# Optimization experiments

Measured on AMD Instinct MI355X. Metric: run time of the kernel, lower is better.

## Reference

```python
import jax, jax.numpy as jnp
import numpy as np

N = 16384
K = 16

def _w(k, shape):
    return jax.random.normal(k, shape, jnp.float32) * 0.05

def setup_inputs() -> dict:
    key = jax.random.key(0)
    ks = jax.random.split(key, 20)
    return {
        "img_feat": jax.random.normal(ks[0], (1, 32, N), jnp.float32),
        "cloud": jax.random.uniform(ks[1], (1, N, 3), jnp.float32),
        "conv1_w": _w(ks[2], (64, 32)),   "conv1_b": _w(ks[3], (64,)),
        "conv2_w": _w(ks[4], (128, 64)),  "conv2_b": _w(ks[5], (128,)),
        "psconv1_w": _w(ks[6], (256, 128)), "psconv1_b": _w(ks[7], (256,)),
        "psconv2_w": _w(ks[8], (128, 256)), "psconv2_b": _w(ks[9], (128,)),
        "pconv1_w": _w(ks[10], (64, 3)),  "pconv1_b": _w(ks[11], (64,)),
        "pconv2_w": _w(ks[12], (128, 64)),"pconv2_b": _w(ks[13], (128,)),
        "final_w": _w(ks[14], (32, 416)), "final_b": _w(ks[15], (32,)),
        "topk": K,
    }

def reference(img_feat, cloud, conv1_w, conv1_b, conv2_w, conv2_b,
              psconv1_w, psconv1_b, psconv2_w, psconv2_b,
              pconv1_w, pconv1_b, pconv2_w, pconv2_b,
              final_w, final_b, topk):
    lrelu = lambda x: jax.nn.leaky_relu(x, 0.01)
    pts = cloud[0]            # [N,3]  (module assumes bs=1)
    imf = img_feat[0].T       # [N,32]
    # point MLP: pconv1 -> lrelu -> pconv2 (Conv1d kernel=1 == per-point linear)
    cf = lrelu(pts @ pconv1_w.T + pconv1_b) @ pconv2_w.T + pconv2_b  # [N,128]
    # KNN: k smallest euclidean distances (self included)
    sq = jnp.sum(pts * pts, axis=-1)                 # [N]
    d2 = sq[:, None] + sq[None, :] - 2.0 * (pts @ pts.T)  # [N,N]
    _, idx = jax.lax.top_k(-d2, topk)                # [N,K]
    nb_pts = pts[idx]                                # [N,K,3]
    dist = jnp.sqrt(jnp.maximum(jnp.sum((pts[:, None, :] - nb_pts) ** 2, -1), 1e-12))
    wgt = jax.nn.softmax(-dist, axis=1)              # [N,K]
    nb_img = imf[idx]                                # [N,K,32]
    nb_cf = cf[idx]                                  # [N,K,128]
    sf = lrelu(nb_img @ conv1_w.T + conv1_b) @ conv2_w.T + conv2_b         # [N,K,128]
    sfp = lrelu(nb_cf @ psconv1_w.T + psconv1_b) @ psconv2_w.T + psconv2_b # [N,K,128]
    sf = jnp.max(sf * wgt[:, :, None], axis=1)       # weighted max-pool -> [N,128]
    sfp = jnp.max(sfp * wgt[:, :, None], axis=1)     # [N,128]
    final = jnp.concatenate([sfp, imf, sf, cf], axis=1)  # [N,416]
    out = lrelu(final) @ final_w.T + final_b         # [N,32]
    return out.T[None]                               # [1,32,N]
```

## Files before the change

kernel.cpp:

```cpp
#include <hip/hip_runtime.h>
#include <math.h>

#define N 16384
#define KNN 16
#define G 16
#define NCELL 4096

typedef __attribute__((ext_vector_type(8))) short bf16x8;
typedef __attribute__((ext_vector_type(4))) float f32x4;
typedef unsigned short ushort_t;
typedef unsigned long long u64;

__device__ __forceinline__ float lrelu(float a) { return a > 0.f ? a : 0.01f * a; }

__device__ __forceinline__ ushort_t f2bf(float f) {
  unsigned u = __float_as_uint(f);
  u += 0x7FFF + ((u >> 16) & 1);
  return (ushort_t)(u >> 16);
}
__device__ __forceinline__ float bf2f(ushort_t h) {
  return __uint_as_float((unsigned)h << 16);
}
__device__ __forceinline__ int lanerank(u64 mask) {
  return __builtin_amdgcn_mbcnt_hi((unsigned)(mask >> 32),
         __builtin_amdgcn_mbcnt_lo((unsigned)mask, 0));
}
__device__ __forceinline__ int cellof(float x) {
  int c = (int)(x * (float)G);
  return c < 0 ? 0 : (c > G - 1 ? G - 1 : c);
}

#define PPB 64
__global__ __launch_bounds__(256) void prepw_kernel(
    const float* __restrict__ img, const float* __restrict__ cloud,
    const float* __restrict__ p1w, const float* __restrict__ p1b,
    const float* __restrict__ p2w, const float* __restrict__ p2b,
    const float* __restrict__ ps1w, const float* __restrict__ ps2w,
    const float* __restrict__ c1w, const float* __restrict__ c2w,
    const float* __restrict__ fw,
    float4* __restrict__ pts4, ushort_t* __restrict__ cfh,
    ushort_t* __restrict__ imfh,
    ushort_t* __restrict__ w1h, ushort_t* __restrict__ w2h,
    ushort_t* __restrict__ c1h, ushort_t* __restrict__ c2h,
    float* __restrict__ fwp2, int* __restrict__ count) {
  int t = threadIdx.x;
  if (blockIdx.x >= 256) {
    int e = (blockIdx.x - 256) * 256 + t;
    if (e < 32768) w1h[e] = f2bf(ps1w[e]);
    else if (e < 65536) w2h[e - 32768] = f2bf(ps2w[e - 32768]);
    else if (e < 67584) c1h[e - 65536] = f2bf(c1w[e - 65536]);
    else if (e < 75776) c2h[e - 67584] = f2bf(c2w[e - 67584]);
    else if (e < 89088) {
      int e2 = e - 75776;
      int j4 = e2 >> 7, r2 = e2 & 127;
      int ch = r2 >> 2, sub = r2 & 3;
      fwp2[e2] = fw[ch * 416 + j4 * 4 + sub];
    }
    return;
  }
  __shared__ alignas(16) float w2t[64 * 132];
  __shared__ alignas(16) float hs[PPB * 68];
  __shared__ alignas(16) float w1s[192];
  __shared__ alignas(16) float b1s[64];
  __shared__ alignas(16) float b2s[128];
  __shared__ float ptmp[PPB * 3];
  __shared__ float psx[PPB], psy[PPB], psz[PPB];
  int pb = blockIdx.x * PPB;

  for (int e = t; e < 128 * 64; e += 256) {
    int ch = e >> 6, k = e & 63;
    w2t[k * 132 + ch] = p2w[e];
  }
  if (t < 192) w1s[t] = p1w[t];
  if (t < 64) b1s[t] = p1b[t];
  if (t < 128) b2s[t] = p2b[t];
  if (t < PPB * 3) ptmp[t] = cloud[pb * 3 + t];
  __syncthreads();
  if (t < PPB) {
    float x = ptmp[t * 3], y = ptmp[t * 3 + 1], z = ptmp[t * 3 + 2];
    psx[t] = x; psy[t] = y; psz[t] = z;
    pts4[pb + t] = make_float4(x, y, z, x * x + y * y + z * z);
    int cid = ((cellof(z) << 4) | cellof(y)) << 4 | cellof(x);
    atomicAdd(&count[cid], 1);
  }
  for (int e = t; e < 32 * PPB; e += 256) {
    int c = e >> 6, p = e & 63;
    imfh[(size_t)(pb + p) * 32 + c] = f2bf(img[(size_t)c * N + pb + p]);
  }
  __syncthreads();
  for (int e = t; e < PPB * 64; e += 256) {
    int pt_ = e >> 6, ch = e & 63;
    float a = b1s[ch] + psx[pt_] * w1s[ch * 3] + psy[pt_] * w1s[ch * 3 + 1] +
              psz[pt_] * w1s[ch * 3 + 2];
    hs[pt_ * 68 + ch] = lrelu(a);
  }
  __syncthreads();
  for (int e = t; e < PPB * 32; e += 256) {
    int pt_ = e >> 5, c4 = (e & 31) << 2;
    float4 acc = *(const float4*)&b2s[c4];
    const float* hrow = &hs[pt_ * 68];
    #pragma unroll
    for (int k = 0; k < 64; k += 4) {
      float4 h4 = *(const float4*)&hrow[k];
      float4 w0 = *(const float4*)&w2t[(k + 0) * 132 + c4];
      float4 w1_ = *(const float4*)&w2t[(k + 1) * 132 + c4];
      float4 w2_ = *(const float4*)&w2t[(k + 2) * 132 + c4];
      float4 w3 = *(const float4*)&w2t[(k + 3) * 132 + c4];
      acc.x = fmaf(h4.x, w0.x, fmaf(h4.y, w1_.x, fmaf(h4.z, w2_.x, fmaf(h4.w, w3.x, acc.x))));
      acc.y = fmaf(h4.x, w0.y, fmaf(h4.y, w1_.y, fmaf(h4.z, w2_.y, fmaf(h4.w, w3.y, acc.y))));
      acc.z = fmaf(h4.x, w0.z, fmaf(h4.y, w1_.z, fmaf(h4.z, w2_.z, fmaf(h4.w, w3.z, acc.z))));
      acc.w = fmaf(h4.x, w0.w, fmaf(h4.y, w1_.w, fmaf(h4.z, w2_.w, fmaf(h4.w, w3.w, acc.w))));
    }
    unsigned lo = (unsigned)f2bf(acc.x) | ((unsigned)f2bf(acc.y) << 16);
    unsigned hi = (unsigned)f2bf(acc.z) | ((unsigned)f2bf(acc.w) << 16);
    *(uint2*)&cfh[(size_t)(pb + pt_) * 128 + c4] = make_uint2(lo, hi);
  }
}

__global__ __launch_bounds__(256) void scan_kernel(
    const int* __restrict__ count, int* __restrict__ cellStart,
    int* __restrict__ cellofs) {
  __shared__ int part[256];
  int t = threadIdx.x;
  int local[16];
  int s = 0;
  #pragma unroll
  for (int j = 0; j < 16; ++j) { local[j] = s; s += count[t * 16 + j]; }
  part[t] = s;
  __syncthreads();
  for (int off = 1; off < 256; off <<= 1) {
    int v = (t >= off) ? part[t - off] : 0;
    __syncthreads();
    part[t] += v;
    __syncthreads();
  }
  int base = part[t] - s;
  #pragma unroll
  for (int j = 0; j < 16; ++j) {
    int v = base + local[j];
    cellStart[t * 16 + j] = v;
    cellofs[t * 16 + j] = v;
  }
  if (t == 255) cellStart[NCELL] = part[255];
}

__global__ __launch_bounds__(256) void scatter_kernel(
    const float4* __restrict__ pts4, int* __restrict__ cellofs,
    float4* __restrict__ spts) {
  int p = blockIdx.x * 256 + threadIdx.x;
  float4 v = pts4[p];
  int cid = ((cellof(v.z) << 4) | cellof(v.y)) << 4 | cellof(v.x);
  int pos = atomicAdd(&cellofs[cid], 1);
  spts[pos] = make_float4(v.x, v.y, v.z, __int_as_float(p));
}

#define NB_LD 136
#define S1_LD 264
#define NI_LD 40
#define H1_LD 72
__global__ __launch_bounds__(256) void ymlp_kernel(
    const ushort_t* __restrict__ cfh, const ushort_t* __restrict__ imfh,
    const ushort_t* __restrict__ w1h, const float* __restrict__ b1,
    const ushort_t* __restrict__ w2h, const float* __restrict__ b2,
    const ushort_t* __restrict__ c1h, const float* __restrict__ c1b,
    const ushort_t* __restrict__ c2h, const float* __restrict__ c2b,
    ushort_t* __restrict__ ycf, ushort_t* __restrict__ yimg) {
  __shared__ ushort_t nb[64 * NB_LD];
  __shared__ ushort_t s1[64 * S1_LD];
  int t = threadIdx.x;
  int w = t >> 6, lane = t & 63;
  int col = lane & 15, quad = lane >> 4;

  if (blockIdx.x < 256) {
    int pbase = blockIdx.x * 64;
    for (int e = t; e < 1024; e += 256) {
      int row = e >> 4, c8 = (e & 15) << 3;
      *(uint4*)&nb[row * NB_LD + c8] =
          *(const uint4*)&cfh[(size_t)(pbase + row) * 128 + c8];
    }
    __syncthreads();
    f32x4 acc1[4][4];
    #pragma unroll
    for (int tt = 0; tt < 4; ++tt)
      #pragma unroll
      for (int p = 0; p < 4; ++p) acc1[tt][p] = (f32x4){0.f, 0.f, 0.f, 0.f};
    for (int k0 = 0; k0 < 128; k0 += 32) {
      bf16x8 a[4];
      #pragma unroll
      for (int p = 0; p < 4; ++p)
        a[p] = *(const bf16x8*)&nb[(p * 16 + col) * NB_LD + k0 + quad * 8];
      #pragma unroll
      for (int tt = 0; tt < 4; ++tt) {
        int n = w * 64 + tt * 16 + col;
        bf16x8 b = *(const bf16x8*)&w1h[n * 128 + k0 + quad * 8];
        #pragma unroll
        for (int p = 0; p < 4; ++p)
          acc1[tt][p] = __builtin_amdgcn_mfma_f32_16x16x32_bf16(a[p], b, acc1[tt][p], 0, 0, 0);
      }
    }
    #pragma unroll
    for (int tt = 0; tt < 4; ++tt) {
      int n = w * 64 + tt * 16 + col;
      float bb = b1[n];
      #pragma unroll
      for (int p = 0; p < 4; ++p)
        #pragma unroll
        for (int r = 0; r < 4; ++r)
          s1[(p * 16 + quad * 4 + r) * S1_LD + n] = f2bf(lrelu(acc1[tt][p][r] + bb));
    }
    __syncthreads();
    f32x4 acc2[2][4];
    #pragma unroll
    for (int tt = 0; tt < 2; ++tt)
      #pragma unroll
      for (int p = 0; p < 4; ++p) acc2[tt][p] = (f32x4){0.f, 0.f, 0.f, 0.f};
    for (int k0 = 0; k0 < 256; k0 += 32) {
      bf16x8 a[4];
      #pragma unroll
      for (int p = 0; p < 4; ++p)
        a[p] = *(const bf16x8*)&s1[(p * 16 + col) * S1_LD + k0 + quad * 8];
      #pragma unroll
      for (int tt = 0; tt < 2; ++tt) {
        int n = w * 32 + tt * 16 + col;
        bf16x8 b = *(const bf16x8*)&w2h[n * 256 + k0 + quad * 8];
        #pragma unroll
        for (int p = 0; p < 4; ++p)
          acc2[tt][p] = __builtin_amdgcn_mfma_f32_16x16x32_bf16(a[p], b, acc2[tt][p], 0, 0, 0);
      }
    }
    #pragma unroll
    for (int tt = 0; tt < 2; ++tt) {
      int n = w * 32 + tt * 16 + col;
      float bb = b2[n];
      #pragma unroll
      for (int p = 0; p < 4; ++p)
        #pragma unroll
        for (int r = 0; r < 4; ++r)
          ycf[(size_t)(pbase + p * 16 + quad * 4 + r) * 128 + n] =
              f2bf(acc2[tt][p][r] + bb);
    }
  } else {
    int pbase = (blockIdx.x - 256) * 64;
    ushort_t* nbi = nb;
    ushort_t* h1 = s1;
    {
      int row = t >> 2, c8 = (t & 3) << 3;
      *(uint4*)&nbi[row * NI_LD + c8] =
          *(const uint4*)&imfh[(size_t)(pbase + row) * 32 + c8];
    }
    __syncthreads();
    {
      f32x4 accA[4];
      #pragma unroll
      for (int p = 0; p < 4; ++p) accA[p] = (f32x4){0.f, 0.f, 0.f, 0.f};
      int n = w * 16 + col;
      bf16x8 b = *(const bf16x8*)&c1h[n * 32 + quad * 8];
      #pragma unroll
      for (int p = 0; p < 4; ++p) {
        bf16x8 a = *(const bf16x8*)&nbi[(p * 16 + col) * NI_LD + quad * 8];
        accA[p] = __builtin_amdgcn_mfma_f32_16x16x32_bf16(a, b, accA[p], 0, 0, 0);
      }
      __syncthreads();
      float bb = c1b[n];
      #pragma unroll
      for (int p = 0; p < 4; ++p)
        #pragma unroll
        for (int r = 0; r < 4; ++r)
          h1[(p * 16 + quad * 4 + r) * H1_LD + n] = f2bf(lrelu(accA[p][r] + bb));
    }
    __syncthreads();
    f32x4 acc2[2][4];
    #pragma unroll
    for (int tt = 0; tt < 2; ++tt)
      #pragma unroll
      for (int p = 0; p < 4; ++p) acc2[tt][p] = (f32x4){0.f, 0.f, 0.f, 0.f};
    for (int k0 = 0; k0 < 64; k0 += 32) {
      bf16x8 a[4];
      #pragma unroll
      for (int p = 0; p < 4; ++p)
        a[p] = *(const bf16x8*)&h1[(p * 16 + col) * H1_LD + k0 + quad * 8];
      #pragma unroll
      for (int tt = 0; tt < 2; ++tt) {
        int n = w * 32 + tt * 16 + col;
        bf16x8 b = *(const bf16x8*)&c2h[n * 64 + k0 + quad * 8];
        #pragma unroll
        for (int p = 0; p < 4; ++p)
          acc2[tt][p] = __builtin_amdgcn_mfma_f32_16x16x32_bf16(a[p], b, acc2[tt][p], 0, 0, 0);
      }
    }
    #pragma unroll
    for (int tt = 0; tt < 2; ++tt) {
      int n = w * 32 + tt * 16 + col;
      float bb = c2b[n];
      #pragma unroll
      for (int p = 0; p < 4; ++p)
        #pragma unroll
        for (int r = 0; r < 4; ++r)
          yimg[(size_t)(pbase + p * 16 + quad * 4 + r) * 128 + n] =
              f2bf(acc2[tt][p][r] + bb);
    }
  }
}

__device__ __forceinline__ u64 bsort64(u64 v, int lane) {
  #pragma unroll
  for (int k = 2; k <= 64; k <<= 1) {
    #pragma unroll
    for (int j = k >> 1; j >= 1; j >>= 1) {
      u64 p = __shfl_xor(v, j);
      bool keepmin = (((lane & j) == 0) == ((lane & k) == 0));
      u64 mn = v < p ? v : p;
      u64 mx = v < p ? p : v;
      v = keepmin ? mn : mx;
    }
  }
  return v;
}

__device__ __forceinline__ u64 bclean64(u64 v, int lane) {
  #pragma unroll
  for (int j = 32; j >= 1; j >>= 1) {
    u64 p = __shfl_xor(v, j);
    u64 mn = v < p ? v : p;
    u64 mx = v < p ? p : v;
    v = ((lane & j) == 0) ? mn : mx;
  }
  return v;
}

__device__ __forceinline__ u64 compact_topk(u64* buf, int& cnt, int lane, float& tau) {
  u64 v = (lane < cnt) ? buf[lane] : ~0ULL;
  v = bsort64(v, lane);
  if (cnt > 64) {
    u64 t = (64 + lane < cnt) ? buf[64 + lane] : ~0ULL;
    t = bsort64(t, lane);
    t = __shfl_xor(t, 63);
    v = (t < v) ? t : v;
    v = bclean64(v, lane);
  }
  if (lane < 16) buf[lane] = v;
  cnt = 16;
  u64 k15 = __shfl(v, 15);
  tau = __uint_as_float((unsigned)(k15 >> 32));
  if (!(tau == tau)) tau = INFINITY;
  return v;
}

__device__ __forceinline__ float tadj(float tau, float qw) {
  float a = tau - qw;
  return a + fabsf(a) * 2e-7f + 1e-35f;
}

__global__ __launch_bounds__(256) void knng_kernel(
    const float4* __restrict__ pts4, const float4* __restrict__ spts,
    const int* __restrict__ cellStart,
    const ushort_t* __restrict__ ycf, const ushort_t* __restrict__ yimg,
    const ushort_t* __restrict__ cfh, const ushort_t* __restrict__ imfh,
    const float* __restrict__ fwp2, const float* __restrict__ fb,
    float* __restrict__ out) {
  __shared__ u64 sbuf[4][128];
  __shared__ alignas(16) float feat[4][416];
  int t = threadIdx.x;
  int wv = t >> 6, lane = t & 63;
  int wid = blockIdx.x * 4 + wv;
  u64* buf = sbuf[wv];

  float4 q = pts4[wid];
  float q2x = -2.f * q.x, q2y = -2.f * q.y, q2z = -2.f * q.z, qw = q.w;
  int cx = cellof(q.x), cy = cellof(q.y), cz = cellof(q.z);
  float tau = INFINITY;
  u64 vres;

  for (int r = 1;; ++r) {
    int lx = max(cx - r, 0), hx = min(cx + r, G - 1);
    int ly = max(cy - r, 0), hy = min(cy + r, G - 1);
    int lz = max(cz - r, 0), hz = min(cz + r, G - 1);
    int ny = hy - ly + 1, nz = hz - lz + 1, nruns = ny * nz;
    int cnt = 0;
    float ta = tadj(tau, qw);

    for (int rb = 0; rb < nruns; rb += 64) {
      int ln = rb + lane;
      int rs = 0, rc = 0;
      if (ln < nruns) {
        int z = lz + ln / ny, y = ly + ln % ny;
        int row = ((z << 4) | y) << 4;
        rs = cellStart[row + lx];
        rc = cellStart[row + hx + 1] - rs;
      }
      int off = rc;
      #pragma unroll
      for (int d = 1; d < 64; d <<= 1) {
        int v = __shfl_up(off, d);
        if (lane >= d) off += v;
      }
      int T = __shfl(off, 63);
      off -= rc;

      for (int cb = 0; cb < T; cb += 64) {
        int rk = cb + lane;
        int j = 0;
        #pragma unroll
        for (int step = 32; step; step >>= 1) {
          int nj = j + step;
          int onj = __shfl(off, nj & 63);
          if (nj < 64 && onj <= rk) j = nj;
        }
        int src = __shfl(rs, j) + rk - __shfl(off, j);
        bool valid = rk < T;
        if (!valid) src = 0;
        float4 c = spts[src];
        float cw = fmaf(c.z, c.z, fmaf(c.y, c.y, c.x * c.x));
        float d2 = fmaf(q2x, c.x, fmaf(q2y, c.y, fmaf(q2z, c.z, cw)));
        bool pass = valid && (d2 <= ta);
        u64 mask = __ballot(pass);
        if (mask) {
          if (pass) {
            int oid = __float_as_int(c.w);
            u64 key = ((u64)__float_as_uint(fmaxf(d2 + qw, 0.f)) << 32) | (unsigned)oid;
            buf[cnt + lanerank(mask)] = key;
          }
          cnt += __popcll(mask);
          if (cnt > 64) {
            compact_topk(buf, cnt, lane, tau);
            ta = tadj(tau, qw);
          }
        }
      }
    }
    u64 v = compact_topk(buf, cnt, lane, tau);
    float cl = INFINITY;
    if (lx > 0)     cl = fminf(cl, q.x - (float)lx / (float)G);
    if (hx < G - 1) cl = fminf(cl, (float)(hx + 1) / (float)G - q.x);
    if (ly > 0)     cl = fminf(cl, q.y - (float)ly / (float)G);
    if (hy < G - 1) cl = fminf(cl, (float)(hy + 1) / (float)G - q.y);
    if (lz > 0)     cl = fminf(cl, q.z - (float)lz / (float)G);
    if (hz < G - 1) cl = fminf(cl, (float)(hz + 1) / (float)G - q.z);
    bool full = (lx == 0 && hx == G - 1 && ly == 0 && hy == G - 1 &&
                 lz == 0 && hz == G - 1);
    if (full || tau * 1.00002f <= cl * cl) { vres = v; break; }
  }

  int myid = (lane < KNN) ? (int)(unsigned)(vres & 0xffffffffULL) : 0;
  float mywg = 0.f;
  {
    float4 c = pts4[myid];
    float dx = q.x - c.x, dy = q.y - c.y, dz = q.z - c.z;
    float dist = sqrtf(fmaxf(dx * dx + dy * dy + dz * dz, 1e-12f));
    float md = (lane < KNN) ? dist : INFINITY;
    #pragma unroll
    for (int off = 1; off < KNN; off <<= 1) md = fminf(md, __shfl_xor(md, off));
    float e = expf(md - dist);
    float se = (lane < KNN) ? e : 0.f;
    #pragma unroll
    for (int off = 1; off < KNN; off <<= 1) se += __shfl_xor(se, off);
    mywg = e / se;
  }

  int pid = wid;
  int ksub = lane >> 4, c8 = lane & 15;
  float vimf = (lane < 32) ? bf2f(imfh[(size_t)pid * 32 + lane]) : 0.f;
  unsigned vcf = *(const unsigned*)&cfh[(size_t)pid * 128 + lane * 2];

  float a0[8], a1[8];
  #pragma unroll
  for (int j = 0; j < 8; ++j) { a0[j] = -INFINITY; a1[j] = -INFINITY; }
  #pragma unroll
  for (int kk = 0; kk < 4; ++kk) {
    int k = kk * 4 + ksub;
    int id = __shfl(myid, k);
    float wg = __shfl(mywg, k);
    uint4 v = *(const uint4*)&ycf[(size_t)id * 128 + c8 * 8];
    uint4 u = *(const uint4*)&yimg[(size_t)id * 128 + c8 * 8];
    unsigned vv[4] = {v.x, v.y, v.z, v.w};
    unsigned uu[4] = {u.x, u.y, u.z, u.w};
    #pragma unroll
    for (int h = 0; h < 4; ++h) {
      a0[h * 2]     = fmaxf(a0[h * 2],     bf2f((ushort_t)(vv[h] & 0xffff)) * wg);
      a0[h * 2 + 1] = fmaxf(a0[h * 2 + 1], bf2f((ushort_t)(vv[h] >> 16)) * wg);
      a1[h * 2]     = fmaxf(a1[h * 2],     bf2f((ushort_t)(uu[h] & 0xffff)) * wg);
      a1[h * 2 + 1] = fmaxf(a1[h * 2 + 1], bf2f((ushort_t)(uu[h] >> 16)) * wg);
    }
  }
  #pragma unroll
  for (int j = 0; j < 8; ++j) {
    a0[j] = fmaxf(a0[j], __shfl_xor(a0[j], 16));
    a0[j] = fmaxf(a0[j], __shfl_xor(a0[j], 32));
    a1[j] = fmaxf(a1[j], __shfl_xor(a1[j], 16));
    a1[j] = fmaxf(a1[j], __shfl_xor(a1[j], 32));
  }
  if (lane < 16) {
    #pragma unroll
    for (int j = 0; j < 8; ++j) {
      feat[wv][c8 * 8 + j] = lrelu(a0[j]);
      feat[wv][160 + c8 * 8 + j] = lrelu(a1[j]);
    }
  }
  if (lane < 32) feat[wv][128 + lane] = lrelu(vimf);
  feat[wv][288 + lane * 2] = lrelu(bf2f((ushort_t)(vcf & 0xffff)));
  feat[wv][288 + lane * 2 + 1] = lrelu(bf2f((ushort_t)(vcf >> 16)));

  int ch = lane & 31, half = lane >> 5;
  float acc = half ? 0.f : fb[ch];
  const float* wr = fwp2 + (half * 52) * 128 + ch * 4;
  const float* fr = &feat[wv][half * 208];
  #pragma unroll 4
  for (int j4 = 0; j4 < 52; ++j4) {
    float4 w4 = *(const float4*)(wr + j4 * 128);
    float4 f4 = *(const float4*)(fr + j4 * 4);
    acc = fmaf(f4.x, w4.x, fmaf(f4.y, w4.y, fmaf(f4.z, w4.z, fmaf(f4.w, w4.w, acc))));
  }
  acc += __shfl_xor(acc, 32);
  if (lane < 32) out[(size_t)ch * N + pid] = acc;
}

extern "C" void kernel_launch(void* const* d_in, const int* in_sizes, int n_in,
                              void* d_out, int out_size, void* d_ws, size_t ws_size,
                              hipStream_t stream) {
  const float* img   = (const float*)d_in[0];
  const float* cloud = (const float*)d_in[1];
  const float* c1w   = (const float*)d_in[2];
  const float* c1b   = (const float*)d_in[3];
  const float* c2w   = (const float*)d_in[4];
  const float* c2b   = (const float*)d_in[5];
  const float* ps1w  = (const float*)d_in[6];
  const float* ps1b  = (const float*)d_in[7];
  const float* ps2w  = (const float*)d_in[8];
  const float* ps2b  = (const float*)d_in[9];
  const float* p1w   = (const float*)d_in[10];
  const float* p1b   = (const float*)d_in[11];
  const float* p2w   = (const float*)d_in[12];
  const float* p2b   = (const float*)d_in[13];
  const float* fw    = (const float*)d_in[14];
  const float* fb    = (const float*)d_in[15];
  float* out = (float*)d_out;

  char* ws = (char*)d_ws;
  float4*   pts4  = (float4*)(ws + 0);
  ushort_t* cfh   = (ushort_t*)(ws + 262144);
  ushort_t* imfh  = (ushort_t*)(ws + 4456448);
  ushort_t* w1h   = (ushort_t*)(ws + 7602176);
  ushort_t* w2h   = (ushort_t*)(ws + 7667712);
  ushort_t* c1h   = (ushort_t*)(ws + 7733248);
  ushort_t* c2h   = (ushort_t*)(ws + 7737344);
  ushort_t* ycf   = (ushort_t*)(ws + 7753472);
  ushort_t* yimg  = (ushort_t*)(ws + 11947776);
  float4*   spts  = (float4*)(ws + 16142080);
  int*      cellStart = (int*)(ws + 16404224);
  int*      cellofs   = (int*)(ws + 16436992);
  int*      count     = (int*)(ws + 16453376);
  float*    fwp2      = (float*)(ws + 16469760);

  hipMemsetAsync(count, 0, NCELL * sizeof(int), stream);
  prepw_kernel<<<604, 256, 0, stream>>>(img, cloud, p1w, p1b, p2w, p2b,
                                        ps1w, ps2w, c1w, c2w, fw,
                                        pts4, cfh, imfh, w1h, w2h, c1h, c2h,
                                        fwp2, count);
  scan_kernel<<<1, 256, 0, stream>>>(count, cellStart, cellofs);
  scatter_kernel<<<64, 256, 0, stream>>>(pts4, cellofs, spts);
  ymlp_kernel<<<512, 256, 0, stream>>>(cfh, imfh, w1h, ps1b, w2h, ps2b,
                                       c1h, c1b, c2h, c2b, ycf, yimg);
  knng_kernel<<<N / 4, 256, 0, stream>>>(pts4, spts, cellStart,
                                         ycf, yimg, cfh, imfh,
                                         fwp2, fb, out);
}
```

Before: 190.2 us.

## Reorder point features into spatial cell order for local neighbor gathers

```diff
diff --git a/kernel.cpp b/kernel.cpp
--- a/kernel.cpp
+++ b/kernel.cpp
@@ -145,13 +145,30 @@
 }
 
 __global__ __launch_bounds__(256) void scatter_kernel(
-    const float4* __restrict__ pts4, int* __restrict__ cellofs,
-    float4* __restrict__ spts) {
-  int p = blockIdx.x * 256 + threadIdx.x;
+    const float4* __restrict__ pts4, const ushort_t* __restrict__ cfh,
+    const ushort_t* __restrict__ imfh, int* __restrict__ cellofs,
+    float4* __restrict__ spts, ushort_t* __restrict__ cfs,
+    ushort_t* __restrict__ imfs) {
+  __shared__ int sposl[256];
+  int t = threadIdx.x;
+  int pbase = blockIdx.x * 256;
+  int p = pbase + t;
   float4 v = pts4[p];
   int cid = ((cellof(v.z) << 4) | cellof(v.y)) << 4 | cellof(v.x);
   int pos = atomicAdd(&cellofs[cid], 1);
+  sposl[t] = pos;
   spts[pos] = make_float4(v.x, v.y, v.z, __int_as_float(p));
+  __syncthreads();
+  for (int e = t; e < 256 * 16; e += 256) {
+    int row = e >> 4, part = e & 15;
+    *(uint4*)&cfs[(size_t)sposl[row] * 128 + part * 8] =
+        *(const uint4*)&cfh[(size_t)(pbase + row) * 128 + part * 8];
+  }
+  for (int e = t; e < 256 * 4; e += 256) {
+    int row = e >> 2, part = e & 3;
+    *(uint4*)&imfs[(size_t)sposl[row] * 32 + part * 8] =
+        *(const uint4*)&imfh[(size_t)(pbase + row) * 32 + part * 8];
+  }
 }
 
 #define NB_LD 136
@@ -159,7 +176,7 @@
 #define NI_LD 40
 #define H1_LD 72
 __global__ __launch_bounds__(256) void ymlp_kernel(
-    const ushort_t* __restrict__ cfh, const ushort_t* __restrict__ imfh,
+    const ushort_t* __restrict__ cfs, const ushort_t* __restrict__ imfs,
     const ushort_t* __restrict__ w1h, const float* __restrict__ b1,
     const ushort_t* __restrict__ w2h, const float* __restrict__ b2,
     const ushort_t* __restrict__ c1h, const float* __restrict__ c1b,
@@ -176,7 +193,7 @@
     for (int e = t; e < 1024; e += 256) {
       int row = e >> 4, c8 = (e & 15) << 3;
       *(uint4*)&nb[row * NB_LD + c8] =
-          *(const uint4*)&cfh[(size_t)(pbase + row) * 128 + c8];
+          *(const uint4*)&cfs[(size_t)(pbase + row) * 128 + c8];
     }
     __syncthreads();
     f32x4 acc1[4][4];
@@ -246,7 +263,7 @@
     {
       int row = t >> 2, c8 = (t & 3) << 3;
       *(uint4*)&nbi[row * NI_LD + c8] =
-          *(const uint4*)&imfh[(size_t)(pbase + row) * 32 + c8];
+          *(const uint4*)&imfs[(size_t)(pbase + row) * 32 + c8];
     }
     __syncthreads();
     {
@@ -313,17 +330,6 @@
       u64 mx = v < p ? p : v;
       v = keepmin ? mn : mx;
     }
-  }
-  return v;
-}
-
-__device__ __forceinline__ u64 bclean64(u64 v, int lane) {
-  #pragma unroll
-  for (int j = 32; j >= 1; j >>= 1) {
-    u64 p = __shfl_xor(v, j);
-    u64 mn = v < p ? v : p;
-    u64 mx = v < p ? p : v;
-    v = ((lane & j) == 0) ? mn : mx;
   }
   return v;
 }
@@ -336,12 +342,18 @@
     t = bsort64(t, lane);
     t = __shfl_xor(t, 63);
     v = (t < v) ? t : v;
-    v = bclean64(v, lane);
+    #pragma unroll
+    for (int j = 32; j >= 1; j >>= 1) {
+      u64 p = __shfl_xor(v, j);
+      u64 mn = v < p ? v : p;
+      u64 mx = v < p ? p : v;
+      v = ((lane & j) == 0) ? mn : mx;
+    }
   }
   if (lane < 16) buf[lane] = v;
   cnt = 16;
   u64 k15 = __shfl(v, 15);
-  tau = __uint_as_float((unsigned)(k15 >> 32));
+  tau = __uint_as_float((unsigned)(k15 >> 28));
   if (!(tau == tau)) tau = INFINITY;
   return v;
 }
@@ -352,21 +364,23 @@
 }
 
 __global__ __launch_bounds__(256) void knng_kernel(
-    const float4* __restrict__ pts4, const float4* __restrict__ spts,
-    const int* __restrict__ cellStart,
+    const float4* __restrict__ spts, const int* __restrict__ cellStart,
     const ushort_t* __restrict__ ycf, const ushort_t* __restrict__ yimg,
-    const ushort_t* __restrict__ cfh, const ushort_t* __restrict__ imfh,
+    const ushort_t* __restrict__ cfs, const ushort_t* __restrict__ imfs,
     const float* __restrict__ fwp2, const float* __restrict__ fb,
     float* __restrict__ out) {
   __shared__ u64 sbuf[4][128];
   __shared__ alignas(16) float feat[4][416];
   int t = threadIdx.x;
   int wv = t >> 6, lane = t & 63;
-  int wid = blockIdx.x * 4 + wv;
+  int sb = (blockIdx.x & 7) * 512 + (blockIdx.x >> 3);
+  int s = sb * 4 + wv;
   u64* buf = sbuf[wv];
 
-  float4 q = pts4[wid];
-  float q2x = -2.f * q.x, q2y = -2.f * q.y, q2z = -2.f * q.z, qw = q.w;
+  float4 q = spts[s];
+  int oidq = __float_as_int(q.w);
+  float qw = fmaf(q.z, q.z, fmaf(q.y, q.y, q.x * q.x));
+  float q2x = -2.f * q.x, q2y = -2.f * q.y, q2z = -2.f * q.z;
   int cx = cellof(q.x), cy = cellof(q.y), cz = cellof(q.z);
   float tau = INFINITY;
   u64 vres;
@@ -416,8 +430,9 @@
         u64 mask = __ballot(pass);
         if (mask) {
           if (pass) {
-            int oid = __float_as_int(c.w);
-            u64 key = ((u64)__float_as_uint(fmaxf(d2 + qw, 0.f)) << 32) | (unsigned)oid;
+            unsigned oid = (unsigned)__float_as_int(c.w);
+            u64 key = ((u64)__float_as_uint(fmaxf(d2 + qw, 0.f)) << 28) |
+                      ((u64)oid << 14) | (unsigned)src;
             buf[cnt + lanerank(mask)] = key;
           }
           cnt += __popcll(mask);
@@ -441,10 +456,10 @@
     if (full || tau * 1.00002f <= cl * cl) { vres = v; break; }
   }
 
-  int myid = (lane < KNN) ? (int)(unsigned)(vres & 0xffffffffULL) : 0;
+  int myspos = (lane < KNN) ? (int)(vres & 0x3FFF) : 0;
   float mywg = 0.f;
   {
-    float4 c = pts4[myid];
+    float4 c = spts[myspos];
     float dx = q.x - c.x, dy = q.y - c.y, dz = q.z - c.z;
     float dist = sqrtf(fmaxf(dx * dx + dy * dy + dz * dz, 1e-12f));
     float md = (lane < KNN) ? dist : INFINITY;
@@ -457,10 +472,9 @@
     mywg = e / se;
   }
 
-  int pid = wid;
   int ksub = lane >> 4, c8 = lane & 15;
-  float vimf = (lane < 32) ? bf2f(imfh[(size_t)pid * 32 + lane]) : 0.f;
-  unsigned vcf = *(const unsigned*)&cfh[(size_t)pid * 128 + lane * 2];
+  float vimf = (lane < 32) ? bf2f(imfs[(size_t)s * 32 + lane]) : 0.f;
+  unsigned vcf = *(const unsigned*)&cfs[(size_t)s * 128 + lane * 2];
 
   float a0[8], a1[8];
   #pragma unroll
@@ -468,7 +482,7 @@
   #pragma unroll
   for (int kk = 0; kk < 4; ++kk) {
     int k = kk * 4 + ksub;
-    int id = __shfl(myid, k);
+    int id = __shfl(myspos, k);
     float wg = __shfl(mywg, k);
     uint4 v = *(const uint4*)&ycf[(size_t)id * 128 + c8 * 8];
     uint4 u = *(const uint4*)&yimg[(size_t)id * 128 + c8 * 8];
@@ -511,7 +525,7 @@
     acc = fmaf(f4.x, w4.x, fmaf(f4.y, w4.y, fmaf(f4.z, w4.z, fmaf(f4.w, w4.w, acc))));
   }
   acc += __shfl_xor(acc, 32);
-  if (lane < 32) out[(size_t)ch * N + pid] = acc;
+  if (lane < 32) out[(size_t)ch * N + oidq] = acc;
 }
 
 extern "C" void kernel_launch(void* const* d_in, const int* in_sizes, int n_in,
@@ -539,17 +553,19 @@
   float4*   pts4  = (float4*)(ws + 0);
   ushort_t* cfh   = (ushort_t*)(ws + 262144);
   ushort_t* imfh  = (ushort_t*)(ws + 4456448);
-  ushort_t* w1h   = (ushort_t*)(ws + 7602176);
-  ushort_t* w2h   = (ushort_t*)(ws + 7667712);
-  ushort_t* c1h   = (ushort_t*)(ws + 7733248);
-  ushort_t* c2h   = (ushort_t*)(ws + 7737344);
-  ushort_t* ycf   = (ushort_t*)(ws + 7753472);
-  ushort_t* yimg  = (ushort_t*)(ws + 11947776);
-  float4*   spts  = (float4*)(ws + 16142080);
-  int*      cellStart = (int*)(ws + 16404224);
-  int*      cellofs   = (int*)(ws + 16436992);
-  int*      count     = (int*)(ws + 16453376);
-  float*    fwp2      = (float*)(ws + 16469760);
+  ushort_t* w1h   = (ushort_t*)(ws + 5505024);
+  ushort_t* w2h   = (ushort_t*)(ws + 5570560);
+  ushort_t* c1h   = (ushort_t*)(ws + 5636096);
+  ushort_t* c2h   = (ushort_t*)(ws + 5640192);
+  ushort_t* ycf   = (ushort_t*)(ws + 5656576);
+  ushort_t* yimg  = (ushort_t*)(ws + 9850880);
+  float4*   spts  = (float4*)(ws + 14045184);
+  ushort_t* cfs   = (ushort_t*)(ws + 14307328);
+  ushort_t* imfs  = (ushort_t*)(ws + 18501632);
+  int*      cellStart = (int*)(ws + 19550208);
+  int*      cellofs   = (int*)(ws + 19582976);
+  int*      count     = (int*)(ws + 19599360);
+  float*    fwp2      = (float*)(ws + 19615744);
 
   hipMemsetAsync(count, 0, NCELL * sizeof(int), stream);
   prepw_kernel<<<604, 256, 0, stream>>>(img, cloud, p1w, p1b, p2w, p2b,
@@ -557,10 +573,10 @@
                                         pts4, cfh, imfh, w1h, w2h, c1h, c2h,
                                         fwp2, count);
   scan_kernel<<<1, 256, 0, stream>>>(count, cellStart, cellofs);
-  scatter_kernel<<<64, 256, 0, stream>>>(pts4, cellofs, spts);
-  ymlp_kernel<<<512, 256, 0, stream>>>(cfh, imfh, w1h, ps1b, w2h, ps2b,
+  scatter_kernel<<<64, 256, 0, stream>>>(pts4, cfh, imfh, cellofs,
+                                         spts, cfs, imfs);
+  ymlp_kernel<<<512, 256, 0, stream>>>(cfs, imfs, w1h, ps1b, w2h, ps2b,
                                        c1h, c1b, c2h, c2b, ycf, yimg);
-  knng_kernel<<<N / 4, 256, 0, stream>>>(pts4, spts, cellStart,
-                                         ycf, yimg, cfh, imfh,
-                                         fwp2, fb, out);
-}
+  knng_kernel<<<N / 4, 256, 0, stream>>>(spts, cellStart, ycf, yimg,
+                                         cfs, imfs, fwp2, fb, out);
+}
```

Result: no change. 192.3 us (+1.1%).
